# Kernel optimization log

Measured on AMD Instinct MI355X. Metric: run time of the kernel, lower is better.

Reference implementation:

```python
import jax, jax.numpy as jnp
import numpy as np

CAP = 15.0
EPS = 1e-6
NUM_HEADS = 16
HEAD_DIM = 64

def _rmsnorm(x, w):
    xf = x.astype(jnp.float32)
    var = jnp.mean(xf * xf, axis=-1, keepdims=True)
    return w * (xf * jax.lax.rsqrt(var + EPS)).astype(x.dtype)

def _gate(g):
    # sigmoid(soft_cap(g)) with cap 15
    return jax.nn.sigmoid(CAP * jnp.tanh(g / CAP))

def setup_inputs() -> dict:
    key = jax.random.key(0)
    ks = jax.random.split(key, 4)
    B, S, D = 4, 2048, 1024
    H, Dh = NUM_HEADS, HEAD_DIM
    return {
        "x": jax.random.normal(ks[0], (B, S, D), jnp.float32),
        "hidden_state": jnp.zeros((B, H, Dh, Dh), jnp.float32),
        "w_rms": jnp.ones((D,), jnp.float32),
        "w_qkv": jax.random.normal(ks[1], (D, 3 * H * Dh), jnp.float32) * 0.02,
        "w_gate": jax.random.normal(ks[2], (D, 3 * H), jnp.float32) * 0.02,
        "w_out": jax.random.normal(ks[3], (D, D), jnp.float32) * 0.02,
    }

def reference(x, hidden_state, w_rms, w_qkv, w_gate, w_out):
    B, S, D = x.shape
    H, Dh = NUM_HEADS, HEAD_DIM
    residual = x
    xn = _rmsnorm(x, w_rms)
    qkv = (xn @ w_qkv).reshape(B, S, 3, H, Dh)
    q, k, v = qkv[:, :, 0], qkv[:, :, 1], qkv[:, :, 2]  # [B,S,H,Dh]
    gates = _gate((xn @ w_gate).reshape(B, S, 3, H))
    i_g, f_g, o_g = gates[:, :, 0], gates[:, :, 1], gates[:, :, 2]  # [B,S,H]

    # time-major for scan: [S,B,H,...]
    def tm(a):
        return jnp.moveaxis(a, 1, 0)

    def step(state, inp):
        qt, kt, vt, it, ft, ot = inp  # [B,H,Dh]/[B,H]
        kv = kt[..., :, None] * vt[..., None, :]            # [B,H,Dh,Dh]
        state = ft[..., None, None] * state + it[..., None, None] * kv
        h = jnp.einsum('bhd,bhde->bhe', qt, state) * ot[..., None]
        return state, h

    _, h_seq = jax.lax.scan(step, hidden_state,
                            (tm(q), tm(k), tm(v), tm(i_g), tm(f_g), tm(o_g)))
    out = jnp.moveaxis(h_seq, 0, 1).reshape(B, S, H * Dh) @ w_out
    return residual + out
```

## Files before the change

### kernel.cpp

```cpp
#include <hip/hip_runtime.h>
#include <math.h>

typedef unsigned short u16;
typedef unsigned int   u32;
typedef __bf16 bf16x8 __attribute__((ext_vector_type(8)));
typedef float  f32x4  __attribute__((ext_vector_type(4)));

#define NBATCH 4
#define SEQ    2048
#define DIM    1024
#define NH     16
#define BH     64
#define NC     32
#define ROWS   8192
#define N1     3328

__device__ __forceinline__ u16 f2bf(float f) {
  u32 u = __builtin_bit_cast(u32, f);
  u32 r = u + 0x7fffu + ((u >> 16) & 1u);
  return (u16)(r >> 16);
}
__device__ __forceinline__ float bf2f(u16 h) {
  return __builtin_bit_cast(float, (u32)h << 16);
}

__device__ __forceinline__ void gl2lds16(const u16* g, u16* l) {
  __builtin_amdgcn_global_load_lds(
      (const __attribute__((address_space(1))) u32*)g,
      (__attribute__((address_space(3))) u32*)l, 16, 0, 0);
}

__global__ __launch_bounds__(256) void prep_w(const float* __restrict__ Wqkv,
                                              const float* __restrict__ Wout,
                                              const float* __restrict__ wg,
                                              u16* __restrict__ BtQkv, u16* __restrict__ BtOut) {
  const int bx = blockIdx.x;
  const int tx = threadIdx.x, ty = threadIdx.y;
  if (bx < 128) {
    const float* W; u16* Bt; int N, n0;
    if (bx < 96) { W = Wqkv; Bt = BtQkv; N = 3072; n0 = bx * 32; }
    else         { W = Wout; Bt = BtOut; N = 1024; n0 = (bx - 96) * 32; }
    const int k0 = blockIdx.y * 32;
    __shared__ float tile[32][33];
    #pragma unroll
    for (int i = 0; i < 4; i++)
      tile[ty + i * 8][tx] = W[(size_t)(k0 + ty + i * 8) * N + n0 + tx];
    __syncthreads();
    #pragma unroll
    for (int i = 0; i < 4; i++)
      Bt[(size_t)(n0 + ty + i * 8) * 1024 + k0 + tx] = f2bf(tile[tx][ty + i * 8]);
  } else {
    const int tid = ty * 32 + tx;
    const int gy = blockIdx.y;
    #pragma unroll
    for (int gg = 0; gg < 8; gg++) {
      const int g = gy * 8 + gg;
      #pragma unroll
      for (int kk = 0; kk < 4; kk++) {
        const int k = kk * 256 + tid;
        u16 v = 0;
        if (g < 48) v = f2bf(wg[(size_t)k * 48 + g]);
        BtQkv[(size_t)(3072 + g) * 1024 + k] = v;
      }
    }
  }
}

__global__ __launch_bounds__(256) void rmsnorm_k(const float* __restrict__ x,
                                                 const float* __restrict__ w,
                                                 u16* __restrict__ xn) {
  const int row = blockIdx.x, tid = threadIdx.x;
  const float4 xv = *(const float4*)&x[(size_t)row * 1024 + tid * 4];
  float ss = xv.x * xv.x + xv.y * xv.y + xv.z * xv.z + xv.w * xv.w;
  #pragma unroll
  for (int off = 32; off > 0; off >>= 1) ss += __shfl_down(ss, off);
  __shared__ float red[4];
  if ((tid & 63) == 0) red[tid >> 6] = ss;
  __syncthreads();
  const float tot = red[0] + red[1] + red[2] + red[3];
  const float scale = rsqrtf(tot * (1.0f / 1024.0f) + 1e-6f);
  const float4 wv = *(const float4*)&w[tid * 4];
  const u16 o0 = f2bf(xv.x * scale * wv.x), o1 = f2bf(xv.y * scale * wv.y);
  const u16 o2 = f2bf(xv.z * scale * wv.z), o3 = f2bf(xv.w * scale * wv.w);
  uint2 ov;
  ov.x = (u32)o0 | ((u32)o1 << 16);
  ov.y = (u32)o2 | ((u32)o3 << 16);
  *(uint2*)&xn[(size_t)row * 1024 + tid * 4] = ov;
}


#define FENCE asm volatile("" ::: "memory")
#define SBAR  do { FENCE; __builtin_amdgcn_s_barrier(); FENCE; } while (0)
#define WAITV4 do { FENCE; asm volatile("s_waitcnt vmcnt(4)" ::: "memory"); } while (0)
#define WAITV0 do { FENCE; asm volatile("s_waitcnt vmcnt(0)" ::: "memory"); } while (0)

#define STAGE_A(BUF, HALF, TILE) do { \
  const u16* s_ = Abase + (size_t)(TILE) * 64 + (size_t)(HALF) * 131072; \
  u16* l_ = &lds[((BUF) * 4 + (HALF)) * 8192 + tid * 8]; \
  gl2lds16(s_, l_); gl2lds16(s_ + 65536, l_ + 4096); \
} while (0)

#define STAGE_B(BUF, HALF, TILE) do { \
  const u16* s_ = Bbase + (size_t)(TILE) * 64 + (size_t)(HALF) * 131072; \
  u16* l_ = &lds[((BUF) * 4 + 2 + (HALF)) * 8192 + tid * 8]; \
  gl2lds16(s_, l_); gl2lds16(s_ + 65536, l_ + 4096); \
} while (0)

#define READ_A(ALDS, MH) do { \
  _Pragma("unroll") \
  for (int mi_ = 0; mi_ < 4; ++mi_) { \
    af[mi_][0] = *(const bf16x8*)((ALDS) + (MH) * 4096 + mi_ * 1024 + co0); \
    af[mi_][1] = *(const bf16x8*)((ALDS) + (MH) * 4096 + mi_ * 1024 + co1); \
  } \
} while (0)

#define READ_B(BLDS, NH) do { \
  _Pragma("unroll") \
  for (int ni_ = 0; ni_ < 2; ++ni_) { \
    bfr[NH][ni_][0] = *(const bf16x8*)((BLDS) + (NH) * 2048 + ni_ * 1024 + co0); \
    bfr[NH][ni_][1] = *(const bf16x8*)((BLDS) + (NH) * 2048 + ni_ * 1024 + co1); \
  } \
} while (0)

#define MFMA16(MH, NH) do { \
  __builtin_amdgcn_s_setprio(1); \
  _Pragma("unroll") \
  for (int mi_ = 0; mi_ < 4; ++mi_) { \
    _Pragma("unroll") \
    for (int ni_ = 0; ni_ < 2; ++ni_) { \
      acc[(MH)*4+mi_][(NH)*2+ni_] = __builtin_amdgcn_mfma_f32_16x16x32_bf16( \
          af[mi_][0], bfr[NH][ni_][0], acc[(MH)*4+mi_][(NH)*2+ni_], 0, 0, 0); \
      acc[(MH)*4+mi_][(NH)*2+ni_] = __builtin_amdgcn_mfma_f32_16x16x32_bf16( \
          af[mi_][1], bfr[NH][ni_][1], acc[(MH)*4+mi_][(NH)*2+ni_], 0, 0, 0); \
    } \
  } \
  __builtin_amdgcn_s_setprio(0); \
} while (0)

#define GITER4(T, FULL) do { \
   \
  READ_A(aLds0, 0); READ_B(bLds0, 0); READ_B(bLds0, 1); \
  STAGE_A(1, 0, 2*(T)+1); STAGE_A(1, 1, 2*(T)+1); \
  SBAR; MFMA16(0, 0); MFMA16(0, 1); SBAR; \
   \
  READ_A(aLds0, 1); \
  if (FULL) { STAGE_B(0, 0, 2*(T)+2); STAGE_B(0, 1, 2*(T)+2); } \
  SBAR; MFMA16(1, 0); MFMA16(1, 1); if (FULL) { WAITV4; } else { WAITV0; } SBAR; \
   \
  READ_A(aLds1, 0); READ_B(bLds1, 0); READ_B(bLds1, 1); \
  if (FULL) { STAGE_A(0, 0, 2*(T)+2); STAGE_A(0, 1, 2*(T)+2); } \
  SBAR; MFMA16(0, 0); MFMA16(0, 1); SBAR; \
   \
  READ_A(aLds1, 1); \
  if (FULL) { STAGE_B(1, 0, 2*(T)+3); STAGE_B(1, 1, 2*(T)+3); } \
  SBAR; MFMA16(1, 0); MFMA16(1, 1); if (FULL) { WAITV4; } SBAR; \
} while (0)

#define CORE_SETUP(AROWBASE, BCOLBASE) \
  const int tid = threadIdx.x; \
  const int lane = tid & 63, wave = tid >> 6; \
  const int q = lane >> 4, m16 = lane & 15; \
  const int wm = wave & 1, wn = wave >> 1; \
  const int sx = m16 & 7; \
  const int co0 = (q ^ sx) * 8; \
  const int co1 = ((4 + q) ^ sx) * 8; \
  const int r0 = tid >> 3, pc = tid & 7; \
  const int lcg = pc ^ (r0 & 7); \
  const u16* Abase = (AROWBASE) + (size_t)r0 * 1024 + lcg * 8; \
  const u16* Bbase = (BCOLBASE) + (size_t)r0 * 1024 + lcg * 8; \
  const u16* aLds0 = &lds[wm * 8192 + m16 * 64]; \
  const u16* aLds1 = aLds0 + 32768; \
  const u16* bLds0 = &lds[16384 + (wn >> 1) * 8192 + ((wn & 1) * 64 + m16) * 64]; \
  const u16* bLds1 = bLds0 + 32768; \
  bf16x8 af[4][2]; \
  bf16x8 bfr[2][2][2]; \
  f32x4 acc[8][4] = {};

#define CORE_RUN16() do { \
  STAGE_A(0, 0, 0); STAGE_A(0, 1, 0); STAGE_B(0, 0, 0); STAGE_B(0, 1, 0); \
  STAGE_B(1, 0, 1); STAGE_B(1, 1, 1); \
  WAITV4; SBAR; \
  _Pragma("unroll 1") \
  for (int t = 0; t < 7; ++t) GITER4(t, 1); \
  GITER4(7, 0); \
} while (0)

__global__ __launch_bounds__(512, 2) void gemm_qkv(const u16* __restrict__ A, const u16* __restrict__ Bt,
                                                   u16* __restrict__ Qb, u16* __restrict__ Kb,
                                                   u16* __restrict__ Vb, float* __restrict__ gates) {
  __shared__ __attribute__((aligned(16))) u16 lds[65536];

  const int g = blockIdx.x;
  const int swz = (g & 7) * 52 + (g >> 3);
  const int bm = swz & 31, bn = swz >> 5;
  const int rowBase = bm * 256, colBase = bn * 256;

  CORE_SETUP(A + (size_t)rowBase * 1024, Bt + (size_t)colBase * 1024);
  CORE_RUN16();

  const int rr = lane >> 2, co = (lane & 3) * 16;
  if (colBase < 3072) {
    const int which = colBase >> 10;
    u16* dstBase = (which == 0) ? Qb : ((which == 1) ? Kb : Vb);
    const int b = rowBase >> 11;
    const int h = ((colBase & 1023) >> 6) + wn;
    const int tRow0 = (rowBase & 2047) + wm * 128;
    u16* headBase = dstBase + ((size_t)(b * 16 + h)) * 2048 * 64;
    u16* scratch = lds + wave * 1024;
    #pragma unroll
    for (int mi = 0; mi < 8; ++mi) {
      #pragma unroll
      for (int bj = 0; bj < 4; ++bj)
        #pragma unroll
        for (int r = 0; r < 4; ++r)
          scratch[(q * 4 + r) * 64 + bj * 16 + m16] = f2bf(acc[mi][bj][r]);
      const uint4 d0 = *(const uint4*)&scratch[rr * 64 + co];
      const uint4 d1 = *(const uint4*)&scratch[rr * 64 + co + 8];
      u16* gp = headBase + (size_t)(tRow0 + mi * 16 + rr) * 64 + co;
      *(uint4*)gp = d0;
      *(uint4*)(gp + 8) = d1;
    }
  } else {
    if (wn == 0) {
      #pragma unroll
      for (int ai = 0; ai < 8; ++ai)
        #pragma unroll
        for (int bj = 0; bj < 3; ++bj)
          #pragma unroll
          for (int r = 0; r < 4; ++r) {
            const int grow = rowBase + wm * 128 + ai * 16 + q * 4 + r;
            const int b = grow >> 11, tt = grow & 2047;
            const float v = acc[ai][bj][r];
            const float gg = 1.0f / (1.0f + __expf(-(15.0f * tanhf(v * (1.0f / 15.0f)))));
            gates[((size_t)bj * 64 + (b * 16 + m16)) * 2048 + tt] = gg;
          }
    }
  }
}

__global__ __launch_bounds__(512, 2) void gemm_out(const u16* __restrict__ A, const u16* __restrict__ Bt,
                                                   const float* __restrict__ resid,
                                                   float* __restrict__ out) {
  __shared__ __attribute__((aligned(16))) u16 lds[65536];

  const int g = blockIdx.x;
  const int swz = (g & 7) * 16 + (g >> 3);
  const int bm = swz & 31, bn = swz >> 5;
  const int rowBase = bm * 256, colBase = bn * 256;

  CORE_SETUP(A + (size_t)rowBase * 1024, Bt + (size_t)colBase * 1024);
  CORE_RUN16();

  const int colW = colBase + (wn >> 1) * 128 + (wn & 1) * 64;
  #pragma unroll
  for (int mi = 0; mi < 8; ++mi)
    #pragma unroll
    for (int bj = 0; bj < 4; ++bj)
      #pragma unroll
      for (int r = 0; r < 4; ++r) {
        const int grow = rowBase + wm * 128 + mi * 16 + q * 4 + r;
        const int gcol = colW + bj * 16 + m16;
        const size_t idx = (size_t)grow * 1024 + gcol;
        out[idx] = acc[mi][bj][r] + resid[idx];
      }
}

__global__ __launch_bounds__(256) void passA_k(const u16* __restrict__ Qb, const u16* __restrict__ Kb,
                                               const u16* __restrict__ Vb,
                                               const float* __restrict__ gates,
                                               float* __restrict__ la,
                                               u16* __restrict__ Mbuf, u16* __restrict__ hseq) {
  __shared__ u16 Ql[64][72], Kl[64][72], KTl[64][72], VTl[64][72], Pl[64][72];
  __shared__ float laS[64], iS[64];
  const int tid = threadIdx.x;
  const int bh = blockIdx.x >> 5, c = blockIdx.x & 31;
  const int lane = tid & 63, w = tid >> 6;
  const int q = lane >> 4, m16 = lane & 15;
  const size_t base = ((size_t)bh * 2048 + c * 64) * 64;
  const int toff = c * 64;

  if (tid < 64) {
    float lg = __logf(gates[(size_t)(64 + bh) * 2048 + toff + tid]);
    #pragma unroll
    for (int off = 1; off < 64; off <<= 1) {
      const float y = __shfl_up(lg, off);
      if (tid >= off) lg += y;
    }
    laS[tid] = lg;
    iS[tid] = gates[(size_t)bh * 2048 + toff + tid];
    la[(size_t)bh * 2048 + toff + tid] = lg;
  }
  __syncthreads();

  {
    const int s = tid >> 2, db = (tid & 3) * 16;
    const float wk = __expf(laS[63] - laS[s]) * iS[s];
    const uint4 q0 = *(const uint4*)&Qb[base + s * 64 + db];
    const uint4 q1 = *(const uint4*)&Qb[base + s * 64 + db + 8];
    *(uint4*)&Ql[s][db] = q0;
    *(uint4*)&Ql[s][db + 8] = q1;
    const uint4 k0 = *(const uint4*)&Kb[base + s * 64 + db];
    const uint4 k1 = *(const uint4*)&Kb[base + s * 64 + db + 8];
    *(uint4*)&Kl[s][db] = k0;
    *(uint4*)&Kl[s][db + 8] = k1;
    u16 ktmp[16];
    *(uint4*)&ktmp[0] = k0;
    *(uint4*)&ktmp[8] = k1;
    #pragma unroll
    for (int j = 0; j < 16; j++) KTl[db + j][s] = f2bf(wk * bf2f(ktmp[j]));
    const uint4 v0 = *(const uint4*)&Vb[base + s * 64 + db];
    const uint4 v1 = *(const uint4*)&Vb[base + s * 64 + db + 8];
    u16 vtmp[16];
    *(uint4*)&vtmp[0] = v0;
    *(uint4*)&vtmp[8] = v1;
    #pragma unroll
    for (int j = 0; j < 16; j++) VTl[db + j][s] = vtmp[j];
  }
  __syncthreads();

  f32x4 pacc[4] = {};
  #pragma unroll
  for (int ks = 0; ks < 2; ks++) {
    const bf16x8 aq = *(const bf16x8*)&Ql[w * 16 + m16][ks * 32 + q * 8];
    #pragma unroll
    for (int ni = 0; ni < 4; ni++) {
      const bf16x8 bk = *(const bf16x8*)&Kl[ni * 16 + m16][ks * 32 + q * 8];
      pacc[ni] = __builtin_amdgcn_mfma_f32_16x16x32_bf16(aq, bk, pacc[ni], 0, 0, 0);
    }
  }
  #pragma unroll
  for (int ni = 0; ni < 4; ni++)
    #pragma unroll
    for (int r = 0; r < 4; r++) {
      const int tt = w * 16 + q * 4 + r, ss = ni * 16 + m16;
      float Wts = 0.0f;
      if (ss <= tt) Wts = __expf(laS[tt] - laS[ss]) * iS[ss];
      Pl[tt][ss] = f2bf(pacc[ni][r] * Wts);
    }
  __syncthreads();

  f32x4 hacc[4] = {}, macc[4] = {};
  #pragma unroll
  for (int ks = 0; ks < 2; ks++) {
    const bf16x8 ap = *(const bf16x8*)&Pl[w * 16 + m16][ks * 32 + q * 8];
    const bf16x8 av = *(const bf16x8*)&VTl[w * 16 + m16][ks * 32 + q * 8];
    #pragma unroll
    for (int ni = 0; ni < 4; ni++) {
      const bf16x8 bv = *(const bf16x8*)&VTl[ni * 16 + m16][ks * 32 + q * 8];
      const bf16x8 bk = *(const bf16x8*)&KTl[ni * 16 + m16][ks * 32 + q * 8];
      hacc[ni] = __builtin_amdgcn_mfma_f32_16x16x32_bf16(ap, bv, hacc[ni], 0, 0, 0);
      macc[ni] = __builtin_amdgcn_mfma_f32_16x16x32_bf16(av, bk, macc[ni], 0, 0, 0);
    }
  }

  __syncthreads();
  #pragma unroll
  for (int ni = 0; ni < 4; ni++)
    #pragma unroll
    for (int r = 0; r < 4; r++) {
      const int tt = w * 16 + q * 4 + r, e = ni * 16 + m16;
      Pl[tt][e] = f2bf(hacc[ni][r]);
      Kl[tt][e] = f2bf(macc[ni][r]);
    }
  __syncthreads();
  {
    const int s = tid >> 2, db = (tid & 3) * 16;
    const int b = bh >> 4, h = bh & 15;
    u16* hp = &hseq[((size_t)b * 2048 + c * 64 + s) * 1024 + h * 64 + db];
    *(uint4*)hp       = *(const uint4*)&Pl[s][db];
    *(uint4*)(hp + 8) = *(const uint4*)&Pl[s][db + 8];
    u16* mp = &Mbuf[(((size_t)bh * 32 + c) * 64 + s) * 64 + db];
    *(uint4*)mp       = *(const uint4*)&Kl[s][db];
    *(uint4*)(mp + 8) = *(const uint4*)&Kl[s][db + 8];
  }
}

__global__ __launch_bounds__(256) void passB_k(u16* __restrict__ Mbuf,
                                               const float* __restrict__ hidden,
                                               const float* __restrict__ la) {
  const int bh = blockIdx.x >> 4;
  const int e = (blockIdx.x & 15) * 256 + threadIdx.x;
  __shared__ float Gs[32];
  if (threadIdx.x < 32)
    Gs[threadIdx.x] = __expf(la[(size_t)bh * 2048 + threadIdx.x * 64 + 63]);
  __syncthreads();
  const int eRow = e >> 6, dCol = e & 63;
  float st = hidden[(size_t)bh * 4096 + dCol * 64 + eRow];
  u16* M = &Mbuf[(size_t)bh * 32 * 4096 + e];
  float m_next = bf2f(M[0]);
  #pragma unroll 4
  for (int c = 0; c < 32; c++) {
    const float m_cur = m_next;
    if (c < 31) m_next = bf2f(M[(size_t)(c + 1) * 4096]);
    M[(size_t)c * 4096] = f2bf(st);
    st = Gs[c] * st + m_cur;
  }
}

__global__ __launch_bounds__(256) void passC_k(const u16* __restrict__ Qb,
                                               const u16* __restrict__ SprevT,
                                               const float* __restrict__ la,
                                               const float* __restrict__ gates,
                                               u16* __restrict__ hseq) {
  __shared__ u16 aQl[64][72], STl[64][72];
  __shared__ float hstage[64][68];
  __shared__ float laS[64], oS[64];
  const int tid = threadIdx.x;
  const int bh = blockIdx.x >> 5, c = blockIdx.x & 31;
  const int lane = tid & 63, w = tid >> 6;
  const int q = lane >> 4, m16 = lane & 15;
  const size_t base = ((size_t)bh * 2048 + c * 64) * 64;
  const int toff = c * 64;
  if (tid < 64) {
    laS[tid] = la[(size_t)bh * 2048 + toff + tid];
    oS[tid] = gates[(size_t)(128 + bh) * 2048 + toff + tid];
  }
  {
    const int s = tid >> 2, db = (tid & 3) * 16;
    *(uint4*)&aQl[s][db]     = *(const uint4*)&Qb[base + s * 64 + db];
    *(uint4*)&aQl[s][db + 8] = *(const uint4*)&Qb[base + s * 64 + db + 8];
    const u16* SpT = &SprevT[((size_t)bh * 32 + c) * 4096];
    *(uint4*)&STl[s][db]     = *(const uint4*)&SpT[s * 64 + db];
    *(uint4*)&STl[s][db + 8] = *(const uint4*)&SpT[s * 64 + db + 8];
  }
  __syncthreads();
  f32x4 acc[4] = {};
  #pragma unroll
  for (int ks = 0; ks < 2; ks++) {
    const bf16x8 a = *(const bf16x8*)&aQl[w * 16 + m16][ks * 32 + q * 8];
    #pragma unroll
    for (int ni = 0; ni < 4; ni++) {
      const bf16x8 bb = *(const bf16x8*)&STl[ni * 16 + m16][ks * 32 + q * 8];
      acc[ni] = __builtin_amdgcn_mfma_f32_16x16x32_bf16(a, bb, acc[ni], 0, 0, 0);
    }
  }
  #pragma unroll
  for (int ni = 0; ni < 4; ni++)
    #pragma unroll
    for (int r = 0; r < 4; r++)
      hstage[w * 16 + q * 4 + r][ni * 16 + m16] = acc[ni][r];
  __syncthreads();
  {
    const int s = tid >> 2, db = (tid & 3) * 16;
    const int b = bh >> 4, h = bh & 15;
    const float a_t = __expf(laS[s]);
    const float o = oS[s];
    u16* hp = &hseq[((size_t)b * 2048 + c * 64 + s) * 1024 + h * 64 + db];
    uint4 h0 = *(const uint4*)hp, h1 = *(const uint4*)(hp + 8);
    u16 hv[16];
    *(uint4*)&hv[0] = h0;
    *(uint4*)&hv[8] = h1;
    float sv[16];
    *(float4*)&sv[0]  = *(const float4*)&hstage[s][db];
    *(float4*)&sv[4]  = *(const float4*)&hstage[s][db + 4];
    *(float4*)&sv[8]  = *(const float4*)&hstage[s][db + 8];
    *(float4*)&sv[12] = *(const float4*)&hstage[s][db + 12];
    u16 ov[16];
    #pragma unroll
    for (int j = 0; j < 16; j++)
      ov[j] = f2bf(o * (bf2f(hv[j]) + a_t * sv[j]));
    *(uint4*)hp       = *(const uint4*)&ov[0];
    *(uint4*)(hp + 8) = *(const uint4*)&ov[8];
  }
}

extern "C" void kernel_launch(void* const* d_in, const int* in_sizes, int n_in,
                              void* d_out, int out_size, void* d_ws, size_t ws_size,
                              hipStream_t stream) {
  (void)in_sizes; (void)n_in; (void)out_size; (void)ws_size;
  const float* x      = (const float*)d_in[0];
  const float* hidden = (const float*)d_in[1];
  const float* w_rms  = (const float*)d_in[2];
  const float* w_qkv  = (const float*)d_in[3];
  const float* w_gate = (const float*)d_in[4];
  const float* w_out  = (const float*)d_in[5];
  float* out = (float*)d_out;

  char* p = (char*)d_ws;
  u16* wqkvT = (u16*)p;  p += (size_t)N1 * 1024 * 2;
  u16* woutT = (u16*)p;  p += (size_t)1024 * 1024 * 2;
  u16* xn    = (u16*)p;  p += (size_t)ROWS * 1024 * 2;
  u16* Qb    = (u16*)p;  p += (size_t)BH * 2048 * 64 * 2;
  u16* Kb    = (u16*)p;  p += (size_t)BH * 2048 * 64 * 2;
  u16* Vb    = (u16*)p;  p += (size_t)BH * 2048 * 64 * 2;
  float* gates = (float*)p; p += (size_t)3 * BH * 2048 * 4;
  float* la    = (float*)p; p += (size_t)BH * 2048 * 4;
  u16* Mbuf  = (u16*)p;  p += (size_t)BH * NC * 4096 * 2;
  u16* hseq  = (u16*)p;  p += (size_t)ROWS * 1024 * 2;

  prep_w<<<dim3(129, 32), dim3(32, 8), 0, stream>>>(w_qkv, w_out, w_gate, wqkvT, woutT);
  rmsnorm_k<<<ROWS, 256, 0, stream>>>(x, w_rms, xn);
  gemm_qkv<<<416, 512, 0, stream>>>(xn, wqkvT, Qb, Kb, Vb, gates);
  passA_k<<<BH * NC, 256, 0, stream>>>(Qb, Kb, Vb, gates, la, Mbuf, hseq);
  passB_k<<<BH * 16, 256, 0, stream>>>(Mbuf, hidden, la);
  passC_k<<<BH * NC, 256, 0, stream>>>(Qb, Mbuf, la, gates, hseq);
  gemm_out<<<128, 512, 0, stream>>>(hseq, woutT, x, out);
}
```

Baseline: 255.8 us.

## Merge weight prep with RMSNorm and retile output GEMM to 128x256 blocks

The RMSNorm kernel and the weight transpose/convert kernel become one launch, with block ranges dispatched by block index. The output projection GEMM moves from 128 blocks of 256x256 tiles to 256 blocks of 128x256 tiles, using a new staging/MFMA pipeline with smaller LDS and fewer accumulators. This aims to fill more of the 256 CUs and drop one kernel launch. The cost is that each block reuses its loaded data less.

```diff
diff --git a/kernel.cpp b/kernel.cpp
--- a/kernel.cpp
+++ b/kernel.cpp
@@ -30,68 +30,71 @@
       (__attribute__((address_space(3))) u32*)l, 16, 0, 0);
 }
 
-__global__ __launch_bounds__(256) void prep_w(const float* __restrict__ Wqkv,
-                                              const float* __restrict__ Wout,
-                                              const float* __restrict__ wg,
-                                              u16* __restrict__ BtQkv, u16* __restrict__ BtOut) {
-  const int bx = blockIdx.x;
-  const int tx = threadIdx.x, ty = threadIdx.y;
-  if (bx < 128) {
-    const float* W; u16* Bt; int N, n0;
-    if (bx < 96) { W = Wqkv; Bt = BtQkv; N = 3072; n0 = bx * 32; }
-    else         { W = Wout; Bt = BtOut; N = 1024; n0 = (bx - 96) * 32; }
-    const int k0 = blockIdx.y * 32;
-    __shared__ float tile[32][33];
-    #pragma unroll
-    for (int i = 0; i < 4; i++)
-      tile[ty + i * 8][tx] = W[(size_t)(k0 + ty + i * 8) * N + n0 + tx];
+__global__ __launch_bounds__(256) void prep_all(const float* __restrict__ x,
+                                                const float* __restrict__ w_rms,
+                                                u16* __restrict__ xn,
+                                                const float* __restrict__ Wqkv,
+                                                const float* __restrict__ Wout,
+                                                const float* __restrict__ wg,
+                                                u16* __restrict__ BtQkv, u16* __restrict__ BtOut) {
+  __shared__ float tile[32][33];
+  __shared__ float red[4];
+  const int bid = blockIdx.x;
+  if (bid < 8192) {
+    const int row = bid, tid = threadIdx.x;
+    const float4 xv = *(const float4*)&x[(size_t)row * 1024 + tid * 4];
+    float ss = xv.x * xv.x + xv.y * xv.y + xv.z * xv.z + xv.w * xv.w;
+    #pragma unroll
+    for (int off = 32; off > 0; off >>= 1) ss += __shfl_down(ss, off);
+    if ((tid & 63) == 0) red[tid >> 6] = ss;
     __syncthreads();
-    #pragma unroll
-    for (int i = 0; i < 4; i++)
-      Bt[(size_t)(n0 + ty + i * 8) * 1024 + k0 + tx] = f2bf(tile[tx][ty + i * 8]);
+    const float tot = red[0] + red[1] + red[2] + red[3];
+    const float scale = rsqrtf(tot * (1.0f / 1024.0f) + 1e-6f);
+    const float4 wv = *(const float4*)&w_rms[tid * 4];
+    const u16 o0 = f2bf(xv.x * scale * wv.x), o1 = f2bf(xv.y * scale * wv.y);
+    const u16 o2 = f2bf(xv.z * scale * wv.z), o3 = f2bf(xv.w * scale * wv.w);
+    uint2 ov;
+    ov.x = (u32)o0 | ((u32)o1 << 16);
+    ov.y = (u32)o2 | ((u32)o3 << 16);
+    *(uint2*)&xn[(size_t)row * 1024 + tid * 4] = ov;
   } else {
-    const int tid = ty * 32 + tx;
-    const int gy = blockIdx.y;
-    #pragma unroll
-    for (int gg = 0; gg < 8; gg++) {
-      const int g = gy * 8 + gg;
+    const int pb = bid - 8192;
+    const int bx = pb % 129, by = pb / 129;
+    const int tx = threadIdx.x & 31, ty = threadIdx.x >> 5;
+    if (bx < 128) {
+      const float* W; u16* Bt; int N, n0;
+      if (bx < 96) { W = Wqkv; Bt = BtQkv; N = 3072; n0 = bx * 32; }
+      else         { W = Wout; Bt = BtOut; N = 1024; n0 = (bx - 96) * 32; }
+      const int k0 = by * 32;
       #pragma unroll
-      for (int kk = 0; kk < 4; kk++) {
-        const int k = kk * 256 + tid;
-        u16 v = 0;
-        if (g < 48) v = f2bf(wg[(size_t)k * 48 + g]);
-        BtQkv[(size_t)(3072 + g) * 1024 + k] = v;
+      for (int i = 0; i < 4; i++)
+        tile[ty + i * 8][tx] = W[(size_t)(k0 + ty + i * 8) * N + n0 + tx];
+      __syncthreads();
+      #pragma unroll
+      for (int i = 0; i < 4; i++)
+        Bt[(size_t)(n0 + ty + i * 8) * 1024 + k0 + tx] = f2bf(tile[tx][ty + i * 8]);
+    } else {
+      const int tid = threadIdx.x;
+      #pragma unroll
+      for (int gg = 0; gg < 8; gg++) {
+        const int g = by * 8 + gg;
+        #pragma unroll
+        for (int kk = 0; kk < 4; kk++) {
+          const int k = kk * 256 + tid;
+          u16 v = 0;
+          if (g < 48) v = f2bf(wg[(size_t)k * 48 + g]);
+          BtQkv[(size_t)(3072 + g) * 1024 + k] = v;
+        }
       }
     }
   }
-}
-
-__global__ __launch_bounds__(256) void rmsnorm_k(const float* __restrict__ x,
-                                                 const float* __restrict__ w,
-                                                 u16* __restrict__ xn) {
-  const int row = blockIdx.x, tid = threadIdx.x;
-  const float4 xv = *(const float4*)&x[(size_t)row * 1024 + tid * 4];
-  float ss = xv.x * xv.x + xv.y * xv.y + xv.z * xv.z + xv.w * xv.w;
-  #pragma unroll
-  for (int off = 32; off > 0; off >>= 1) ss += __shfl_down(ss, off);
-  __shared__ float red[4];
-  if ((tid & 63) == 0) red[tid >> 6] = ss;
-  __syncthreads();
-  const float tot = red[0] + red[1] + red[2] + red[3];
-  const float scale = rsqrtf(tot * (1.0f / 1024.0f) + 1e-6f);
-  const float4 wv = *(const float4*)&w[tid * 4];
-  const u16 o0 = f2bf(xv.x * scale * wv.x), o1 = f2bf(xv.y * scale * wv.y);
-  const u16 o2 = f2bf(xv.z * scale * wv.z), o3 = f2bf(xv.w * scale * wv.w);
-  uint2 ov;
-  ov.x = (u32)o0 | ((u32)o1 << 16);
-  ov.y = (u32)o2 | ((u32)o3 << 16);
-  *(uint2*)&xn[(size_t)row * 1024 + tid * 4] = ov;
 }
 
 
 #define FENCE asm volatile("" ::: "memory")
 #define SBAR  do { FENCE; __builtin_amdgcn_s_barrier(); FENCE; } while (0)
 #define WAITV4 do { FENCE; asm volatile("s_waitcnt vmcnt(4)" ::: "memory"); } while (0)
+#define WAITV2 do { FENCE; asm volatile("s_waitcnt vmcnt(2)" ::: "memory"); } while (0)
 #define WAITV0 do { FENCE; asm volatile("s_waitcnt vmcnt(0)" ::: "memory"); } while (0)
 
 #define STAGE_A(BUF, HALF, TILE) do { \
@@ -238,27 +241,102 @@
   }
 }
 
+
+#define STAGE_AO(BUF, TILE) do { \
+  const u16* s_ = Abase + (size_t)(TILE) * 64; \
+  u16* l_ = &lds[(BUF) * 24576 + tid * 8]; \
+  gl2lds16(s_, l_); gl2lds16(s_ + 65536, l_ + 4096); \
+} while (0)
+
+#define STAGE_BO(BUF, HALF, TILE) do { \
+  const u16* s_ = Bbase + (size_t)(TILE) * 64 + (size_t)(HALF) * 131072; \
+  u16* l_ = &lds[(BUF) * 24576 + 8192 + (HALF) * 8192 + tid * 8]; \
+  gl2lds16(s_, l_); gl2lds16(s_ + 65536, l_ + 4096); \
+} while (0)
+
+#define READ_AO(ALDS) do { \
+  _Pragma("unroll") \
+  for (int mi_ = 0; mi_ < 4; ++mi_) { \
+    af[mi_][0] = *(const bf16x8*)((ALDS) + mi_ * 1024 + co0); \
+    af[mi_][1] = *(const bf16x8*)((ALDS) + mi_ * 1024 + co1); \
+  } \
+} while (0)
+
+#define MFMA16O(NH) do { \
+  __builtin_amdgcn_s_setprio(1); \
+  _Pragma("unroll") \
+  for (int mi_ = 0; mi_ < 4; ++mi_) { \
+    _Pragma("unroll") \
+    for (int ni_ = 0; ni_ < 2; ++ni_) { \
+      acc[mi_][(NH)*2+ni_] = __builtin_amdgcn_mfma_f32_16x16x32_bf16( \
+          af[mi_][0], bfr[NH][ni_][0], acc[mi_][(NH)*2+ni_], 0, 0, 0); \
+      acc[mi_][(NH)*2+ni_] = __builtin_amdgcn_mfma_f32_16x16x32_bf16( \
+          af[mi_][1], bfr[NH][ni_][1], acc[mi_][(NH)*2+ni_], 0, 0, 0); \
+    } \
+  } \
+  __builtin_amdgcn_s_setprio(0); \
+} while (0)
+
+#define GITER_O(T, FULL) do { \
+   READ_AO(aLds0); READ_B(bLds0, 0); \
+         STAGE_BO(1, 0, 2*(T)+1); STAGE_BO(1, 1, 2*(T)+1); \
+         SBAR; MFMA16O(0); SBAR; \
+   READ_B(bLds0, 1); \
+         if (FULL) STAGE_AO(0, 2*(T)+2); \
+         SBAR; MFMA16O(1); if (FULL) { WAITV2; } else { WAITV0; } SBAR; \
+   READ_AO(aLds1); READ_B(bLds1, 0); \
+         if (FULL) { STAGE_BO(0, 0, 2*(T)+2); STAGE_BO(0, 1, 2*(T)+2); } \
+         SBAR; MFMA16O(0); SBAR; \
+   READ_B(bLds1, 1); \
+         if (FULL) STAGE_AO(1, 2*(T)+3); \
+         SBAR; MFMA16O(1); if (FULL) { WAITV2; } SBAR; \
+} while (0)
+
 __global__ __launch_bounds__(512, 2) void gemm_out(const u16* __restrict__ A, const u16* __restrict__ Bt,
                                                    const float* __restrict__ resid,
                                                    float* __restrict__ out) {
-  __shared__ __attribute__((aligned(16))) u16 lds[65536];
+  __shared__ __attribute__((aligned(16))) u16 lds[49152];
 
   const int g = blockIdx.x;
-  const int swz = (g & 7) * 16 + (g >> 3);
-  const int bm = swz & 31, bn = swz >> 5;
-  const int rowBase = bm * 256, colBase = bn * 256;
-
-  CORE_SETUP(A + (size_t)rowBase * 1024, Bt + (size_t)colBase * 1024);
-  CORE_RUN16();
-
-  const int colW = colBase + (wn >> 1) * 128 + (wn & 1) * 64;
-  #pragma unroll
-  for (int mi = 0; mi < 8; ++mi)
+  const int swz = (g & 7) * 32 + (g >> 3);
+  const int bm = swz & 63, bn = swz >> 6;
+  const int rowBase = bm * 128, colBase = bn * 256;
+
+  const int tid = threadIdx.x;
+  const int lane = tid & 63, wave = tid >> 6;
+  const int q = lane >> 4, m16 = lane & 15;
+  const int wm = wave & 1, wn = wave >> 1;
+  const int sx = m16 & 7;
+  const int co0 = (q ^ sx) * 8;
+  const int co1 = ((4 + q) ^ sx) * 8;
+  const int r0 = tid >> 3, pc = tid & 7;
+  const int lcg = pc ^ (r0 & 7);
+  const u16* Abase = A  + (size_t)rowBase * 1024 + (size_t)r0 * 1024 + lcg * 8;
+  const u16* Bbase = Bt + (size_t)colBase * 1024 + (size_t)r0 * 1024 + lcg * 8;
+  const u16* aLds0 = &lds[wm * 4096 + m16 * 64];
+  const u16* aLds1 = aLds0 + 24576;
+  const u16* bLds0 = &lds[8192 + (wn >> 1) * 8192 + ((wn & 1) * 64 + m16) * 64];
+  const u16* bLds1 = bLds0 + 24576;
+  bf16x8 af[4][2];
+  bf16x8 bfr[2][2][2];
+  f32x4 acc[4][4] = {};
+
+  STAGE_AO(0, 0); STAGE_BO(0, 0, 0); STAGE_BO(0, 1, 0);
+  STAGE_AO(1, 1);
+  WAITV2; SBAR;
+
+  #pragma unroll 1
+  for (int t = 0; t < 7; ++t) GITER_O(t, 1);
+  GITER_O(7, 0);
+
+  const int colW = colBase + wn * 64;
+  #pragma unroll
+  for (int mi = 0; mi < 4; ++mi)
     #pragma unroll
     for (int bj = 0; bj < 4; ++bj)
       #pragma unroll
       for (int r = 0; r < 4; ++r) {
-        const int grow = rowBase + wm * 128 + mi * 16 + q * 4 + r;
+        const int grow = rowBase + wm * 64 + mi * 16 + q * 4 + r;
         const int gcol = colW + bj * 16 + m16;
         const size_t idx = (size_t)grow * 1024 + gcol;
         out[idx] = acc[mi][bj][r] + resid[idx];
@@ -488,11 +566,10 @@
   u16* Mbuf  = (u16*)p;  p += (size_t)BH * NC * 4096 * 2;
   u16* hseq  = (u16*)p;  p += (size_t)ROWS * 1024 * 2;
 
-  prep_w<<<dim3(129, 32), dim3(32, 8), 0, stream>>>(w_qkv, w_out, w_gate, wqkvT, woutT);
-  rmsnorm_k<<<ROWS, 256, 0, stream>>>(x, w_rms, xn);
+  prep_all<<<12320, 256, 0, stream>>>(x, w_rms, xn, w_qkv, w_out, w_gate, wqkvT, woutT);
   gemm_qkv<<<416, 512, 0, stream>>>(xn, wqkvT, Qb, Kb, Vb, gates);
   passA_k<<<BH * NC, 256, 0, stream>>>(Qb, Kb, Vb, gates, la, Mbuf, hseq);
   passB_k<<<BH * 16, 256, 0, stream>>>(Mbuf, hidden, la);
   passC_k<<<BH * NC, 256, 0, stream>>>(Qb, Mbuf, la, gates, hseq);
-  gemm_out<<<128, 512, 0, stream>>>(hseq, woutT, x, out);
-}
+  gemm_out<<<256, 512, 0, stream>>>(hseq, woutT, x, out);
+}
```

Result: faster. 241.3 us, median of 4 (-5.7%).
